# Kernel tuning notes

Hardware: AMD Instinct MI355X
Metric: run time of the kernel (lower is better)

The kernel has to match this reference:

```python
import jax, jax.numpy as jnp
import numpy as np

C = 512
K = 3
DIL1 = 1  # dilation[0]
EPS = 1e-9


def _get_padding(kernel_size, dilation=1):
    return (kernel_size * dilation - dilation) // 2


def _upsample2_linear(x):
    # F.interpolate(x, scale_factor=2, mode='linear', align_corners=False)
    # x: [B, C, T] -> [B, C, 2T]
    T = x.shape[-1]
    coord = (jnp.arange(2 * T, dtype=x.dtype) + 0.5) * 0.5 - 0.5
    coord = jnp.maximum(coord, 0.0)  # PyTorch clamps source coord at 0
    i0 = jnp.floor(coord).astype(jnp.int32)
    i1 = jnp.minimum(i0 + 1, T - 1)
    w1 = coord - i0.astype(x.dtype)
    w0 = 1.0 - w1
    return x[..., i0] * w0 + x[..., i1] * w1


def _downsample2_avg(x):
    # AvgPool1d(kernel_size=2, stride=2)
    B, Ch, T = x.shape
    return x.reshape(B, Ch, T // 2, 2).mean(axis=-1)


def _snakebeta_act1d(x, alpha, beta):
    a = jnp.exp(alpha)[None, :, None]
    b = jnp.exp(beta)[None, :, None]
    up = _upsample2_linear(x)
    y = up + (1.0 - jnp.cos(2.0 * a * up)) / (2.0 * b + EPS)
    return _downsample2_avg(y)


def _wn_weight(v, g):
    # weight_norm: w = g * v / ||v||, norm over (in, k) dims per out channel
    norm = jnp.sqrt(jnp.sum(v * v, axis=(1, 2), keepdims=True))
    return g[:, None, None] * v / norm


def _conv1d(x, w, bias, dilation, pad):
    y = jax.lax.conv_general_dilated(
        x, w, window_strides=(1,), padding=[(pad, pad)],
        rhs_dilation=(dilation,), dimension_numbers=('NCH', 'OIH', 'NCH'))
    return y + bias[None, :, None]


def setup_inputs() -> dict:
    key = jax.random.key(0)
    ks = jax.random.split(key, 11)
    B, T = 8, 8192
    x = jax.random.normal(ks[0], (B, C, T), dtype=jnp.float32)
    v1 = jax.random.normal(ks[1], (C, C, K), dtype=jnp.float32) * 0.05
    g1 = jnp.ones((C,), dtype=jnp.float32)
    bias1 = jax.random.normal(ks[2], (C,), dtype=jnp.float32) * 0.01
    v2 = jax.random.normal(ks[3], (C, C, K), dtype=jnp.float32) * 0.05
    g2 = jnp.ones((C,), dtype=jnp.float32)
    bias2 = jax.random.normal(ks[4], (C,), dtype=jnp.float32) * 0.01
    # SnakeBeta logscale params (init 0 in torch; small random for testing)
    alpha1 = jax.random.normal(ks[5], (C,), dtype=jnp.float32) * 0.1
    beta1 = jax.random.normal(ks[6], (C,), dtype=jnp.float32) * 0.1
    alpha2 = jax.random.normal(ks[7], (C,), dtype=jnp.float32) * 0.1
    beta2 = jax.random.normal(ks[8], (C,), dtype=jnp.float32) * 0.1
    return {"x": x, "v1": v1, "g1": g1, "bias1": bias1,
            "v2": v2, "g2": g2, "bias2": bias2,
            "alpha1": alpha1, "beta1": beta1, "alpha2": alpha2, "beta2": beta2}


def reference(x, v1, g1, bias1, v2, g2, bias2, alpha1, beta1, alpha2, beta2):
    pad1 = _get_padding(K, DIL1)
    pad2 = _get_padding(K, 1)
    xt = _snakebeta_act1d(x, alpha1, beta1)
    xt = _conv1d(xt, _wn_weight(v1, g1), bias1, DIL1, pad1)
    xt = _snakebeta_act1d(xt, alpha2, beta2)
    xt = _conv1d(xt, _wn_weight(v2, g2), bias2, 1, pad2)
    return xt + x[:, :, :xt.shape[2]]
```

## Files before the change

### kernel.cpp

```cpp
#include <hip/hip_runtime.h>

typedef unsigned short ushort_t;
typedef __bf16 bf16x8 __attribute__((ext_vector_type(8)));
typedef float f32x4 __attribute__((ext_vector_type(4)));

#define B_  8
#define C_  512
#define T_  8192
#define TP_ 8194

static __device__ __forceinline__ float bf2f(ushort_t u) {
    return __uint_as_float(((unsigned)u) << 16);
}
static __device__ __forceinline__ ushort_t f2bf(float f) {
    unsigned u = __float_as_uint(f);
    unsigned r = (u + 0x7FFFu + ((u >> 16) & 1u)) >> 16;
    return (ushort_t)r;
}

static __device__ __forceinline__ void gl_lds16(const void* g, void* l) {
    __builtin_amdgcn_global_load_lds(
        (const __attribute__((address_space(1))) void*)g,
        (__attribute__((address_space(3))) void*)l, 16, 0, 0);
}

template <int BF> struct In;
template <> struct In<0> {
    static __device__ __forceinline__ float ld(const void* p, size_t i) {
        return ((const float*)p)[i];
    }
};
template <> struct In<1> {
    static __device__ __forceinline__ float ld(const void* p, size_t i) {
        return bf2f(((const ushort_t*)p)[i]);
    }
};

#define P_G1 0
#define P_B1 512
#define P_G2 1024
#define P_B2 1536
#define P_A1 2048
#define P_I1 2560
#define P_A2 3072
#define P_I2 3584

__global__ void param_kernel(const void* g1, const void* bias1, const void* g2, const void* bias2,
                             const void* alpha1, const void* beta1, const void* alpha2, const void* beta2,
                             float* __restrict__ pr, int* __restrict__ flag) {
    int i = threadIdx.x;
    unsigned guard = ((const unsigned*)g1)[0];
    int bf = (guard == 0x3F803F80u) ? 1 : 0;
    if (i == 0) *flag = bf;
    float g1v, b1v, g2v, b2v, a1v, be1v, a2v, be2v;
    if (bf) {
        g1v = In<1>::ld(g1, i);  b1v = In<1>::ld(bias1, i);
        g2v = In<1>::ld(g2, i);  b2v = In<1>::ld(bias2, i);
        a1v = In<1>::ld(alpha1, i); be1v = In<1>::ld(beta1, i);
        a2v = In<1>::ld(alpha2, i); be2v = In<1>::ld(beta2, i);
    } else {
        g1v = In<0>::ld(g1, i);  b1v = In<0>::ld(bias1, i);
        g2v = In<0>::ld(g2, i);  b2v = In<0>::ld(bias2, i);
        a1v = In<0>::ld(alpha1, i); be1v = In<0>::ld(beta1, i);
        a2v = In<0>::ld(alpha2, i); be2v = In<0>::ld(beta2, i);
    }
    pr[P_G1 + i] = g1v;
    pr[P_B1 + i] = b1v;
    pr[P_G2 + i] = g2v;
    pr[P_B2 + i] = b2v;
    pr[P_A1 + i] = __expf(a1v);
    pr[P_I1 + i] = 1.0f / (2.0f * __expf(be1v) + 1e-9f);
    pr[P_A2 + i] = __expf(a2v);
    pr[P_I2 + i] = 1.0f / (2.0f * __expf(be2v) + 1e-9f);
}

__global__ void wn_kernel(const void* __restrict__ v1, const void* __restrict__ v2,
                          const float* __restrict__ pr, const int* __restrict__ flag,
                          ushort_t* __restrict__ W1, ushort_t* __restrict__ W2) {
    int bf = *flag;
    const void* v = blockIdx.y ? v2 : v1;
    float g = pr[(blockIdx.y ? P_G2 : P_G1) + blockIdx.x];
    ushort_t* W = blockIdx.y ? W2 : W1;
    int co = blockIdx.x;
    int tid = threadIdx.x;
    size_t base = (size_t)co * 1536;
    float vals[6];
    float sum = 0.f;
    if (bf) {
        #pragma unroll
        for (int i = 0; i < 6; ++i) {
            float f = In<1>::ld(v, base + tid + i * 256);
            vals[i] = f;
            sum += f * f;
        }
    } else {
        #pragma unroll
        for (int i = 0; i < 6; ++i) {
            float f = In<0>::ld(v, base + tid + i * 256);
            vals[i] = f;
            sum += f * f;
        }
    }
    #pragma unroll
    for (int o = 32; o > 0; o >>= 1) sum += __shfl_down(sum, o, 64);
    __shared__ float red[4];
    if ((tid & 63) == 0) red[tid >> 6] = sum;
    __syncthreads();
    float tot = red[0] + red[1] + red[2] + red[3];
    float scale = g / sqrtf(tot);
    #pragma unroll
    for (int i = 0; i < 6; ++i) {
        int j = tid + i * 256;
        int cin = j / 3, k = j - cin * 3;
        W[(k * C_ + co) * C_ + cin] = f2bf(vals[i] * scale);
    }
}

__global__ void zero_pad_kernel(ushort_t* __restrict__ h) {
    int i = blockIdx.x * 256 + threadIdx.x;
    int b = i >> 10;
    int r = (i >> 9) & 1;
    int c = i & 511;
    h[((size_t)b * TP_ + (r ? (TP_ - 1) : 0)) * C_ + c] = 0;
}

__global__ void act1_kernel(const void* __restrict__ x,
                            const float* __restrict__ pr, const int* __restrict__ flag,
                            ushort_t* __restrict__ h) {
    __shared__ float s[64][65];
    int bf = *flag;
    int c0 = blockIdx.x * 64, t0 = blockIdx.y * 64, b = blockIdx.z;
    int tid = threadIdx.x;
    int cl = tid >> 2, seg = tid & 3;
    int c = c0 + cl;
    float a = pr[P_A1 + c];
    float inv2b = pr[P_I1 + c];
    size_t xbase = ((size_t)b * C_ + c) << 13;
    int tbase = t0 + seg * 16;
    float xv[18];
    if (bf) {
        const ushort_t* xp = (const ushort_t*)x + xbase;
        #pragma unroll
        for (int q = 0; q < 2; ++q) {
            uint4 v = *(const uint4*)(xp + tbase + q * 8);
            const ushort_t* pv = (const ushort_t*)&v;
            #pragma unroll
            for (int j = 0; j < 8; ++j) xv[1 + q * 8 + j] = bf2f(pv[j]);
        }
        xv[0]  = bf2f(xp[max(tbase - 1, 0)]);
        xv[17] = bf2f(xp[min(tbase + 16, T_ - 1)]);
    } else {
        const float* xp = (const float*)x + xbase;
        #pragma unroll
        for (int q = 0; q < 4; ++q) {
            float4 v = *(const float4*)(xp + tbase + q * 4);
            xv[1 + q * 4 + 0] = v.x;
            xv[1 + q * 4 + 1] = v.y;
            xv[1 + q * 4 + 2] = v.z;
            xv[1 + q * 4 + 3] = v.w;
        }
        xv[0]  = xp[max(tbase - 1, 0)];
        xv[17] = xp[min(tbase + 16, T_ - 1)];
    }
    #pragma unroll
    for (int j = 0; j < 16; ++j) {
        float xm = xv[j], xc = xv[j + 1], xp2 = xv[j + 2];
        float u0 = 0.25f * xm + 0.75f * xc;
        float u1 = 0.75f * xc + 0.25f * xp2;
        float s0 = u0 + (1.0f - __cosf(2.0f * a * u0)) * inv2b;
        float s1 = u1 + (1.0f - __cosf(2.0f * a * u1)) * inv2b;
        s[cl][seg * 16 + j] = 0.5f * (s0 + s1);
    }
    __syncthreads();
    int tl = tid >> 2;
    int t = t0 + tl;
    ushort_t* hrow = h + ((size_t)b * TP_ + (t + 1)) * C_ + c0 + seg * 16;
    #pragma unroll
    for (int q = 0; q < 4; ++q) {
        int cb = seg * 16 + q * 4;
        ushort4 w;
        w.x = f2bf(s[cb + 0][tl]);
        w.y = f2bf(s[cb + 1][tl]);
        w.z = f2bf(s[cb + 2][tl]);
        w.w = f2bf(s[cb + 3][tl]);
        *(ushort4*)(hrow + q * 4) = w;
    }
}

__global__ void act2_kernel(const ushort_t* __restrict__ z,
                            const float* __restrict__ pr,
                            ushort_t* __restrict__ h) {
    const int NV = B_ * T_ * (C_ / 8);
    int stride = gridDim.x * blockDim.x;
    for (int v = blockIdx.x * blockDim.x + threadIdx.x; v < NV; v += stride) {
        int c8 = v & 63;
        int t  = (v >> 6) & (T_ - 1);
        int b  = v >> 19;
        int c0 = c8 << 3;
        const ushort_t* zb = z + ((size_t)b << 22);
        uint4 vc = *(const uint4*)(zb + ((size_t)t << 9) + c0);
        uint4 vm = *(const uint4*)(zb + ((size_t)max(t - 1, 0) << 9) + c0);
        uint4 vp = *(const uint4*)(zb + ((size_t)min(t + 1, T_ - 1) << 9) + c0);
        float4 a0 = *(const float4*)(pr + P_A2 + c0);
        float4 a1 = *(const float4*)(pr + P_A2 + c0 + 4);
        float4 i0 = *(const float4*)(pr + P_I2 + c0);
        float4 i1 = *(const float4*)(pr + P_I2 + c0 + 4);
        float av[8] = {a0.x, a0.y, a0.z, a0.w, a1.x, a1.y, a1.z, a1.w};
        float iv[8] = {i0.x, i0.y, i0.z, i0.w, i1.x, i1.y, i1.z, i1.w};
        const ushort_t* pc = (const ushort_t*)&vc;
        const ushort_t* pm = (const ushort_t*)&vm;
        const ushort_t* pp = (const ushort_t*)&vp;
        ushort_t ov[8];
        #pragma unroll
        for (int j = 0; j < 8; ++j) {
            float zc = bf2f(pc[j]), zm = bf2f(pm[j]), zp = bf2f(pp[j]);
            float u0 = 0.25f * zm + 0.75f * zc;
            float u1 = 0.75f * zc + 0.25f * zp;
            float s0 = u0 + (1.0f - __cosf(2.0f * av[j] * u0)) * iv[j];
            float s1 = u1 + (1.0f - __cosf(2.0f * av[j] * u1)) * iv[j];
            ov[j] = f2bf(0.5f * (s0 + s1));
        }
        *(uint4*)(h + ((size_t)b * TP_ + t + 1) * C_ + c0) = *(const uint4*)ov;
    }
}

struct ConvAcc {
    f32x4 acc[4][4];
    int m0, t0, b, l15, qd, wm, wn;
};

static __device__ __forceinline__ void conv_main(const ushort_t* __restrict__ Xt,
                                                 const ushort_t* __restrict__ W,
                                                 ConvAcc& S) {
    __shared__ __align__(16) ushort_t sA[3 * 128 * 32];
    __shared__ __align__(16) ushort_t sB[130 * 32];

    int tid = threadIdx.x;
    int lane = tid & 63, wid = tid >> 6;
    int wbase = tid & ~63;
    S.m0 = blockIdx.x * 128;
    S.t0 = blockIdx.y * 128;
    S.b  = blockIdx.z;
    S.wm = (wid >> 1) * 64;
    S.wn = (wid & 1) * 64;
    S.l15 = lane & 15;
    S.qd  = lane >> 4;
    #pragma unroll
    for (int mi = 0; mi < 4; ++mi)
        #pragma unroll
        for (int ni = 0; ni < 4; ++ni)
            S.acc[mi][ni] = (f32x4){0.f, 0.f, 0.f, 0.f};

    const ushort_t* xb = Xt + ((size_t)S.b * TP_ + S.t0) * C_;

    int hrow = 128 + (tid >> 2), hpart = tid & 3;
    const ushort_t* hbase = xb + (size_t)hrow * C_ + (hpart << 3);
    uint4 hv;
    if (tid < 8) hv = *(const uint4*)hbase;

    for (int ck = 0; ck < 16; ++ck) {
        int cin0 = ck * 32;
        #pragma unroll
        for (int i = 0; i < 6; ++i) {
            int idx = tid + i * 256;
            int tap = idx >> 9;
            int rem = idx & 511;
            int row = rem >> 2, part = rem & 3;
            const ushort_t* gp = W + (((size_t)((tap << 9) + S.m0 + row)) << 9) + cin0 + (part << 3);
            gl_lds16(gp, sA + (size_t)(i * 256 + wbase) * 8);
        }
        #pragma unroll
        for (int i = 0; i < 2; ++i) {
            int idx = tid + i * 256;
            int row = idx >> 2, part = idx & 3;
            const ushort_t* gp = xb + (size_t)row * C_ + cin0 + (part << 3);
            gl_lds16(gp, sB + (size_t)(i * 256 + wbase) * 8);
        }
        if (tid < 8) {
            *(uint4*)(sB + hrow * 32 + (hpart << 3)) = hv;
            if (ck < 15) hv = *(const uint4*)(hbase + cin0 + 32);
        }
        __syncthreads();
        #pragma unroll
        for (int tap = 0; tap < 3; ++tap) {
            bf16x8 af[4], bfr[4];
            #pragma unroll
            for (int mi = 0; mi < 4; ++mi)
                af[mi] = *(const bf16x8*)(sA + tap * 4096 + (S.wm + mi * 16 + S.l15) * 32 + (S.qd << 3));
            #pragma unroll
            for (int ni = 0; ni < 4; ++ni)
                bfr[ni] = *(const bf16x8*)(sB + (S.wn + ni * 16 + S.l15 + tap) * 32 + (S.qd << 3));
            #pragma unroll
            for (int mi = 0; mi < 4; ++mi)
                #pragma unroll
                for (int ni = 0; ni < 4; ++ni)
                    S.acc[mi][ni] = __builtin_amdgcn_mfma_f32_16x16x32_bf16(af[mi], bfr[ni], S.acc[mi][ni], 0, 0, 0);
        }
        __syncthreads();
    }
}

__global__ __launch_bounds__(256) void conv1_kernel(const ushort_t* __restrict__ Xt,
                                                    const ushort_t* __restrict__ W,
                                                    const float* __restrict__ pr,
                                                    ushort_t* __restrict__ out) {
    ConvAcc S;
    conv_main(Xt, W, S);
    ushort_t* ob = out + ((size_t)S.b << 22);
    #pragma unroll
    for (int mi = 0; mi < 4; ++mi) {
        int cb = S.m0 + S.wm + mi * 16 + S.qd * 4;
        float b0 = pr[P_B1 + cb], b1 = pr[P_B1 + cb + 1];
        float b2 = pr[P_B1 + cb + 2], b3 = pr[P_B1 + cb + 3];
        #pragma unroll
        for (int ni = 0; ni < 4; ++ni) {
            int t = S.t0 + S.wn + ni * 16 + S.l15;
            ushort4 w;
            w.x = f2bf(S.acc[mi][ni][0] + b0);
            w.y = f2bf(S.acc[mi][ni][1] + b1);
            w.z = f2bf(S.acc[mi][ni][2] + b2);
            w.w = f2bf(S.acc[mi][ni][3] + b3);
            *(ushort4*)(ob + ((size_t)t << 9) + cb) = w;
        }
    }
}

__global__ __launch_bounds__(256) void conv2_kernel(const ushort_t* __restrict__ Xt,
                                                    const ushort_t* __restrict__ W,
                                                    const float* __restrict__ pr,
                                                    const int* __restrict__ flag,
                                                    const void* __restrict__ xres,
                                                    void* __restrict__ out) {
    int bf = *flag;
    ConvAcc S;
    conv_main(Xt, W, S);
    if (bf) {
        #pragma unroll
        for (int mi = 0; mi < 4; ++mi) {
            int cb = S.m0 + S.wm + mi * 16 + S.qd * 4;
            #pragma unroll
            for (int i = 0; i < 4; ++i) {
                float bi = pr[P_B2 + cb + i];
                size_t rowbase = ((size_t)S.b * C_ + cb + i) << 13;
                #pragma unroll
                for (int ni = 0; ni < 4; ++ni) {
                    int t = S.t0 + S.wn + ni * 16 + S.l15;
                    float val = S.acc[mi][ni][i] + bi + bf2f(((const ushort_t*)xres)[rowbase + t]);
                    ((ushort_t*)out)[rowbase + t] = f2bf(val);
                }
            }
        }
    } else {
        #pragma unroll
        for (int mi = 0; mi < 4; ++mi) {
            int cb = S.m0 + S.wm + mi * 16 + S.qd * 4;
            #pragma unroll
            for (int i = 0; i < 4; ++i) {
                float bi = pr[P_B2 + cb + i];
                size_t rowbase = ((size_t)S.b * C_ + cb + i) << 13;
                #pragma unroll
                for (int ni = 0; ni < 4; ++ni) {
                    int t = S.t0 + S.wn + ni * 16 + S.l15;
                    float val = S.acc[mi][ni][i] + bi + ((const float*)xres)[rowbase + t];
                    ((float*)out)[rowbase + t] = val;
                }
            }
        }
    }
}

extern "C" void kernel_launch(void* const* d_in, const int* in_sizes, int n_in,
                              void* d_out, int out_size, void* d_ws, size_t ws_size,
                              hipStream_t stream) {
    const void* x      = d_in[0];
    const void* v1     = d_in[1];
    const void* g1     = d_in[2];
    const void* bias1  = d_in[3];
    const void* v2     = d_in[4];
    const void* g2     = d_in[5];
    const void* bias2  = d_in[6];
    const void* alpha1 = d_in[7];
    const void* beta1  = d_in[8];
    const void* alpha2 = d_in[9];
    const void* beta2  = d_in[10];

    char* ws = (char*)d_ws;
    const size_t H_BYTES = (size_t)B_ * TP_ * C_ * 2;
    ushort_t* h_buf = (ushort_t*)ws;
    ushort_t* W1n   = (ushort_t*)(ws + H_BYTES);
    ushort_t* W2n   = W1n + 3 * C_ * C_;
    float*    pr    = (float*)(W2n + 3 * C_ * C_);
    int*      flag  = (int*)(pr + 8 * 512);
    ushort_t* z1 = (ushort_t*)d_out;

    param_kernel<<<1, 512, 0, stream>>>(g1, bias1, g2, bias2, alpha1, beta1, alpha2, beta2, pr, flag);
    wn_kernel<<<dim3(C_, 2), 256, 0, stream>>>(v1, v2, pr, flag, W1n, W2n);
    zero_pad_kernel<<<32, 256, 0, stream>>>(h_buf);
    act1_kernel<<<dim3(C_ / 64, T_ / 64, B_), 256, 0, stream>>>(x, pr, flag, h_buf);
    conv1_kernel<<<dim3(C_ / 128, T_ / 128, B_), 256, 0, stream>>>(h_buf, W1n, pr, z1);
    act2_kernel<<<2048, 256, 0, stream>>>(z1, pr, h_buf);
    conv2_kernel<<<dim3(C_ / 128, T_ / 128, B_), 256, 0, stream>>>(h_buf, W2n, pr, flag, x, d_out);
}
```

Baseline: 543.3 us.

## Load conv weights straight to registers and triple-buffer activation tiles in LDS

The shared conv main loop no longer stages weight tiles in LDS. Each wave now loads its A fragments for all three taps directly from global memory into registers. Activation tiles go through a three-slot LDS ring buffer filled two iterations ahead with direct global-to-LDS loads, using hand-placed vmcnt waits and a single barrier per k-step. This is meant to cut LDS traffic and barrier stalls and to overlap memory with MFMA work. The cost is more register pressure and less-coalesced global weight reads that now rely on cache hits.

```diff
diff --git a/kernel.cpp b/kernel.cpp
--- a/kernel.cpp
+++ b/kernel.cpp
@@ -229,11 +229,18 @@
     int m0, t0, b, l15, qd, wm, wn;
 };
 
+#define BUFN 4160
+
+static __device__ __forceinline__ void stage_b(const ushort_t* g0, ushort_t* sq, int wbase) {
+    gl_lds16(g0,           sq + wbase * 8);
+    gl_lds16(g0 + 64 * C_, sq + 2048 + wbase * 8);
+    gl_lds16(g0 + 66 * C_, sq + 2112 + wbase * 8);
+}
+
 static __device__ __forceinline__ void conv_main(const ushort_t* __restrict__ Xt,
                                                  const ushort_t* __restrict__ W,
                                                  ConvAcc& S) {
-    __shared__ __align__(16) ushort_t sA[3 * 128 * 32];
-    __shared__ __align__(16) ushort_t sB[130 * 32];
+    __shared__ __align__(16) ushort_t sB3[3 * BUFN];
 
     int tid = threadIdx.x;
     int lane = tid & 63, wid = tid >> 6;
@@ -252,51 +259,49 @@
             S.acc[mi][ni] = (f32x4){0.f, 0.f, 0.f, 0.f};
 
     const ushort_t* xb = Xt + ((size_t)S.b * TP_ + S.t0) * C_;
-
-    int hrow = 128 + (tid >> 2), hpart = tid & 3;
-    const ushort_t* hbase = xb + (size_t)hrow * C_ + (hpart << 3);
-    uint4 hv;
-    if (tid < 8) hv = *(const uint4*)hbase;
-
+    const ushort_t* gstage = xb + (size_t)(tid >> 2) * C_ + ((tid & 3) << 3);
+    const ushort_t* ab = W + (size_t)(S.m0 + S.wm + S.l15) * C_ + (S.qd << 3);
+
+    stage_b(gstage,      sB3,        wbase);
+    stage_b(gstage + 32, sB3 + BUFN, wbase);
+    asm volatile("s_waitcnt vmcnt(0)" ::: "memory");
+    __builtin_amdgcn_s_barrier();
+    __builtin_amdgcn_sched_barrier(0);
+
+    int p = 0;
     for (int ck = 0; ck < 16; ++ck) {
+        ushort_t* sp = sB3 + p * BUFN;
         int cin0 = ck * 32;
-        #pragma unroll
-        for (int i = 0; i < 6; ++i) {
-            int idx = tid + i * 256;
-            int tap = idx >> 9;
-            int rem = idx & 511;
-            int row = rem >> 2, part = rem & 3;
-            const ushort_t* gp = W + (((size_t)((tap << 9) + S.m0 + row)) << 9) + cin0 + (part << 3);
-            gl_lds16(gp, sA + (size_t)(i * 256 + wbase) * 8);
-        }
-        #pragma unroll
-        for (int i = 0; i < 2; ++i) {
-            int idx = tid + i * 256;
-            int row = idx >> 2, part = idx & 3;
-            const ushort_t* gp = xb + (size_t)row * C_ + cin0 + (part << 3);
-            gl_lds16(gp, sB + (size_t)(i * 256 + wbase) * 8);
-        }
-        if (tid < 8) {
-            *(uint4*)(sB + hrow * 32 + (hpart << 3)) = hv;
-            if (ck < 15) hv = *(const uint4*)(hbase + cin0 + 32);
-        }
-        __syncthreads();
+        bf16x8 af[3][4];
+        #pragma unroll
+        for (int tap = 0; tap < 3; ++tap)
+            #pragma unroll
+            for (int mi = 0; mi < 4; ++mi)
+                af[tap][mi] = *(const bf16x8*)(ab + (size_t)(tap * C_ + mi * 16) * C_ + cin0);
+        __builtin_amdgcn_sched_barrier(0);
+        {
+            int q = p + 2; if (q >= 3) q -= 3;
+            stage_b(gstage + cin0 + 64, sB3 + q * BUFN, wbase);
+        }
+        __builtin_amdgcn_sched_barrier(0);
+        asm volatile("s_waitcnt vmcnt(3)" ::: "memory");
+        __builtin_amdgcn_sched_barrier(0);
         #pragma unroll
         for (int tap = 0; tap < 3; ++tap) {
-            bf16x8 af[4], bfr[4];
-            #pragma unroll
-            for (int mi = 0; mi < 4; ++mi)
-                af[mi] = *(const bf16x8*)(sA + tap * 4096 + (S.wm + mi * 16 + S.l15) * 32 + (S.qd << 3));
+            bf16x8 bfr[4];
             #pragma unroll
             for (int ni = 0; ni < 4; ++ni)
-                bfr[ni] = *(const bf16x8*)(sB + (S.wn + ni * 16 + S.l15 + tap) * 32 + (S.qd << 3));
+                bfr[ni] = *(const bf16x8*)(sp + (S.wn + ni * 16 + S.l15 + tap) * 32 + (S.qd << 3));
             #pragma unroll
             for (int mi = 0; mi < 4; ++mi)
                 #pragma unroll
                 for (int ni = 0; ni < 4; ++ni)
-                    S.acc[mi][ni] = __builtin_amdgcn_mfma_f32_16x16x32_bf16(af[mi], bfr[ni], S.acc[mi][ni], 0, 0, 0);
-        }
-        __syncthreads();
+                    S.acc[mi][ni] = __builtin_amdgcn_mfma_f32_16x16x32_bf16(af[tap][mi], bfr[ni], S.acc[mi][ni], 0, 0, 0);
+        }
+        __builtin_amdgcn_sched_barrier(0);
+        __builtin_amdgcn_s_barrier();
+        __builtin_amdgcn_sched_barrier(0);
+        ++p; if (p >= 3) p -= 3;
     }
 }
 
```

Result: slower. 711.4 us (+31.0%).
